# Kernel tuning notes

Measured on AMD Instinct MI355X. Metric: run time of the kernel, lower is better.

Reference implementation:

```python
import jax, jax.numpy as jnp
import numpy as np

N_BINS = 15
NUM_CLASSES = 16


def _risk_from_H2(u):
    # torch: 0.5*(1 - sqrt(clamp(2*2^-u - 1, min=0)))
    inner = 2.0 * jnp.exp2(-u) - 1.0
    pos = inner > 0.0
    s = jnp.sqrt(jnp.where(pos, inner, 1.0))  # safe sqrt (grad 0 where clamped)
    return 0.5 * (1.0 - jnp.where(pos, s, 0.0))


def setup_inputs() -> dict:
    key = jax.random.key(0)
    k1, k2 = jax.random.split(key)
    N = 4194304
    logits = jax.random.normal(k1, (N, NUM_CLASSES), dtype=jnp.float32)
    labels = jax.random.randint(k2, (N,), 0, NUM_CLASSES)
    return {"logits": logits, "labels": labels}


def reference(logits, labels):
    # logits: [N, C]; labels: [N]
    probs = jax.nn.softmax(logits, axis=-1)                     # [N, C]
    H2 = -jnp.log2((probs * probs).sum(-1) + 1e-12)             # [N]
    err_real = (jnp.argmax(probs, axis=-1) != labels).astype(H2.dtype)  # [N]

    # equal-frequency edges on detached H2 (linear-interp quantiles, as torch.quantile)
    q = jnp.linspace(0.0, 1.0, N_BINS + 1)
    edges = jnp.quantile(jax.lax.stop_gradient(H2), q)
    edges = edges.at[-1].add(1e-6)
    lo, hi = edges[:-1], edges[1:]                              # [n_bins]

    # vectorized replacement of the per-bin Python loop: [n_bins, N] mask
    mask = (H2[None, :] > lo[:, None]) & (H2[None, :] <= hi[:, None])
    maskf = mask.astype(H2.dtype)
    cnt = maskf.sum(-1)                                         # [n_bins]
    safe = jnp.maximum(cnt, 1.0)
    u_bar = (maskf @ H2) / safe                                 # masked means
    err_bar = (maskf @ err_real) / safe
    gaps = jnp.where(cnt > 0.0, jnp.abs(err_bar - _risk_from_H2(u_bar)), 0.0)
    return gaps.mean()
```

## Files before the change

kernel.cpp:

```cpp
#include <hip/hip_runtime.h>

#define L1_BINS 8192
#define L2_BINS 512
#define KEY_MAX 4194303u
#define NH2_BLOCKS 512
#define NREF_BLOCKS 512
#define NBIN_BLOCKS 256

struct Ranks { unsigned int r[32]; };
struct Fracs { float f[16]; };

__global__ __launch_bounds__(256) void k_zero(uint4* __restrict__ p, int n4) {
  int i = blockIdx.x * blockDim.x + threadIdx.x;
  if (i < n4) p[i] = make_uint4(0u, 0u, 0u, 0u);
}

__global__ __launch_bounds__(256) void k_h2(const float* __restrict__ logits,
                                            const int* __restrict__ labels,
                                            unsigned int* __restrict__ keys,
                                            unsigned int* __restrict__ merged,
                                            int n) {
  __shared__ unsigned int lh[L1_BINS];
  for (int i = threadIdx.x; i < L1_BINS; i += blockDim.x) lh[i] = 0u;
  __syncthreads();
  int tid = blockIdx.x * blockDim.x + threadIdx.x;
  int sub = tid & 3;
  int group = tid >> 2;
  int ngroups = (gridDim.x * blockDim.x) >> 2;
  for (int row = group; row < n; row += ngroups) {
    float4 v = reinterpret_cast<const float4*>(logits)[(size_t)row * 4 + sub];
    float m = v.x; int a = 0;
    if (v.y > m) { m = v.y; a = 1; }
    if (v.z > m) { m = v.z; a = 2; }
    if (v.w > m) { m = v.w; a = 3; }
    int gidx = sub * 4 + a;
#pragma unroll
    for (int mask = 1; mask <= 2; mask <<= 1) {
      float om = __shfl_xor(m, mask);
      int oi = __shfl_xor(gidx, mask);
      if (om > m || (om == m && oi < gidx)) { m = om; gidx = oi; }
    }
    float e0 = __expf(v.x - m), e1 = __expf(v.y - m);
    float e2 = __expf(v.z - m), e3 = __expf(v.w - m);
    float Z = e0 + e1 + e2 + e3;
    float S2 = e0 * e0 + e1 * e1 + e2 * e2 + e3 * e3;
#pragma unroll
    for (int mask = 1; mask <= 2; mask <<= 1) {
      Z += __shfl_xor(Z, mask);
      S2 += __shfl_xor(S2, mask);
    }
    if (sub == 0) {
      float r = S2 / (Z * Z) + 1e-12f;
      float h2 = -__log2f(r);
      int ki = (int)(h2 * 1048576.0f);
      unsigned int key = (unsigned int)min(max(ki, 0), (int)KEY_MAX);
      unsigned int err = (gidx != labels[row]) ? 0x80000000u : 0u;
      keys[row] = key | err;
      atomicAdd(&lh[key >> 9], 1u);
    }
  }
  __syncthreads();
  for (int i = threadIdx.x; i < L1_BINS; i += blockDim.x) {
    unsigned int v = lh[i];
    if (v) atomicAdd(&merged[i], v);
  }
}

__global__ void k_select(const unsigned int* __restrict__ hist,
                         unsigned int* __restrict__ selpfx,
                         unsigned int* __restrict__ selrank,
                         float* __restrict__ vout,
                         int nb, int perq, int shift, int last, int first,
                         Ranks rk) {
  int j = blockIdx.x;
  int lane = threadIdx.x;
  const unsigned int* h = hist + (perq ? (size_t)j * (size_t)nb : (size_t)0);
  unsigned int rem = first ? rk.r[j] : selrank[j];
  int base = 0, len = nb;
  while (len > 64) {
    int chunk = (len + 63) >> 6;
    int start = base + lane * chunk;
    int end = base + len;
    unsigned int s = 0;
    for (int t = 0; t < chunk; ++t) {
      int idx = start + t;
      if (idx < end) s += h[idx];
    }
    unsigned int inc = s;
#pragma unroll
    for (int d = 1; d < 64; d <<= 1) {
      unsigned int u = __shfl_up(inc, d);
      if (lane >= d) inc += u;
    }
    unsigned int ex = inc - s;
    bool own = (rem >= ex) && (rem < ex + s);
    unsigned long long bal = __ballot(own);
    int src = __ffsll((long long)bal) - 1;
    unsigned int exs = __shfl(ex, src);
    int nbase = base + src * chunk;
    len = min(chunk, end - nbase);
    base = nbase;
    rem -= exs;
  }
  unsigned int s = (lane < len) ? h[base + lane] : 0u;
  unsigned int inc = s;
#pragma unroll
  for (int d = 1; d < 64; d <<= 1) {
    unsigned int u = __shfl_up(inc, d);
    if (lane >= d) inc += u;
  }
  unsigned int ex = inc - s;
  bool own = (rem >= ex) && (rem < ex + s);
  unsigned long long bal = __ballot(own);
  int src = __ffsll((long long)bal) - 1;
  unsigned int exs = __shfl(ex, src);
  if (lane == 0) {
    unsigned int idx = (unsigned int)(base + src);
    unsigned int pfx = first ? idx : ((selpfx[j] << shift) | idx);
    selpfx[j] = pfx;
    selrank[j] = rem - exs;
    if (last) vout[j] = __uint_as_float(pfx);
  }
}

__global__ __launch_bounds__(256) void k_refine(const unsigned int* __restrict__ keys,
                                                const unsigned int* __restrict__ selpfx,
                                                unsigned int* __restrict__ hist2,
                                                int n) {
  __shared__ unsigned int sp[32];
  if (threadIdx.x < 32) sp[threadIdx.x] = selpfx[threadIdx.x];
  __syncthreads();
  int stride = gridDim.x * blockDim.x;
  for (int i = blockIdx.x * blockDim.x + threadIdx.x; i < n; i += stride) {
    unsigned int key = keys[i] & KEY_MAX;
    unsigned int hi = key >> 9;
    unsigned int sub = key & (L2_BINS - 1);
#pragma unroll
    for (int jj = 0; jj < 32; ++jj) {
      if (hi == sp[jj]) atomicAdd(&hist2[jj * L2_BINS + (int)sub], 1u);
    }
  }
}

__global__ __launch_bounds__(256) void k_bin(const unsigned int* __restrict__ keys,
                                             const float* __restrict__ vp,
                                             float* __restrict__ partials,
                                             unsigned int* __restrict__ done,
                                             float* __restrict__ out, int n,
                                             Fracs fr) {
  __shared__ float sedge[16];
  __shared__ float swacc[4][48];
  __shared__ unsigned int is_last;
  if (threadIdx.x < 16) {
    int i = threadIdx.x;
    unsigned int klo = __float_as_uint(vp[2 * i]);
    unsigned int khi = __float_as_uint(vp[2 * i + 1]);
    float lo = (float)(klo + 1u) * 0x1p-20f;
    float hi = (float)(khi + 1u) * 0x1p-20f;
    float f = fr.f[i];
    float e = lo * (1.0f - f) + hi * f;
    if (i == 15) e += 1e-6f;
    sedge[i] = e;
  }
  __syncthreads();
  float e[16];
#pragma unroll
  for (int j = 0; j < 16; ++j) e[j] = sedge[j];
  float cnt[15], sH[15], sE[15];
#pragma unroll
  for (int b = 0; b < 15; ++b) { cnt[b] = 0.f; sH[b] = 0.f; sE[b] = 0.f; }
  int stride = gridDim.x * blockDim.x;
  for (int i = blockIdx.x * blockDim.x + threadIdx.x; i < n; i += stride) {
    unsigned int kp = keys[i];
    float h = ((float)(kp & KEY_MAX) + 0.5f) * 0x1p-20f;
    float er = (kp & 0x80000000u) ? 1.0f : 0.0f;
    int less = 0;
#pragma unroll
    for (int j = 0; j < 16; ++j) less += (h > e[j]) ? 1 : 0;
    int bin = less - 1;
#pragma unroll
    for (int b = 0; b < 15; ++b) {
      bool m = (bin == b);
      cnt[b] += m ? 1.f : 0.f;
      sH[b] += m ? h : 0.f;
      sE[b] += m ? er : 0.f;
    }
  }
  int wid = threadIdx.x >> 6;
  int lane = threadIdx.x & 63;
#pragma unroll
  for (int b = 0; b < 15; ++b) {
    float c = cnt[b], a = sH[b], s = sE[b];
    for (int off = 32; off > 0; off >>= 1) {
      c += __shfl_xor(c, off);
      a += __shfl_xor(a, off);
      s += __shfl_xor(s, off);
    }
    if (lane == 0) {
      swacc[wid][b] = c;
      swacc[wid][15 + b] = a;
      swacc[wid][30 + b] = s;
    }
  }
  __syncthreads();
  if (threadIdx.x < 45) {
    int v = threadIdx.x;
    float s = swacc[0][v] + swacc[1][v] + swacc[2][v] + swacc[3][v];
    partials[v * NBIN_BLOCKS + blockIdx.x] = s;
  }
  __threadfence();
  if (threadIdx.x == 0)
    is_last = (atomicAdd(done, 1u) == (unsigned int)gridDim.x - 1u) ? 1u : 0u;
  __syncthreads();
  if (is_last && threadIdx.x < 64) {
    __shared__ float sacc[45];
    int l = threadIdx.x;
    for (int v = 0; v < 45; ++v) {
      float s = 0.f;
      for (int b = l; b < NBIN_BLOCKS; b += 64) s += partials[v * NBIN_BLOCKS + b];
      for (int off = 32; off > 0; off >>= 1) s += __shfl_xor(s, off);
      if (l == 0) sacc[v] = s;
    }
    __builtin_amdgcn_s_barrier();
    float g = 0.f;
    if (l < 15) {
      float c = sacc[l], sh = sacc[15 + l], se = sacc[30 + l];
      float safe = fmaxf(c, 1.f);
      float u = sh / safe, eb = se / safe;
      float inner = 2.0f * exp2f(-u) - 1.0f;
      float s = (inner > 0.f) ? sqrtf(inner) : 0.f;
      float risk = 0.5f * (1.0f - s);
      g = (c > 0.f) ? fabsf(eb - risk) : 0.f;
    }
    for (int off = 32; off > 0; off >>= 1) g += __shfl_xor(g, off);
    if (l == 0) out[0] = g * (1.0f / 15.0f);
  }
}

extern "C" void kernel_launch(void* const* d_in, const int* in_sizes, int n_in,
                              void* d_out, int out_size, void* d_ws, size_t ws_size,
                              hipStream_t stream) {
  const float* logits = (const float*)d_in[0];
  const int* labels = (const int*)d_in[1];
  float* out = (float*)d_out;
  int n = in_sizes[1];

  char* ws = (char*)d_ws;
  size_t offKeys = 0;
  size_t offMerged = (size_t)n * 4;
  size_t offH2b = offMerged + (size_t)L1_BINS * 4;
  size_t offDone = offH2b + 32 * L2_BINS * 4;
  size_t zeroEnd = offDone + 16;
  size_t offSelP = zeroEnd;
  size_t offSelR = offSelP + 128;
  size_t offV = offSelR + 128;
  size_t offPart = (offV + 128 + 255) & ~(size_t)255;

  unsigned int* keys = (unsigned int*)(ws + offKeys);
  unsigned int* merged = (unsigned int*)(ws + offMerged);
  unsigned int* hist2 = (unsigned int*)(ws + offH2b);
  unsigned int* done = (unsigned int*)(ws + offDone);
  unsigned int* selp = (unsigned int*)(ws + offSelP);
  unsigned int* selr = (unsigned int*)(ws + offSelR);
  float* vp = (float*)(ws + offV);
  float* part = (float*)(ws + offPart);

  Ranks rk;
  Fracs fr;
  float nm1 = (float)(n - 1);
  for (int i = 0; i < 16; ++i) {
    float q = (i == 15) ? 1.0f : (float)i * (1.0f / 15.0f);
    float idxf = q * nm1;
    float flo = floorf(idxf);
    unsigned int klo = (unsigned int)flo;
    unsigned int khi = (unsigned int)ceilf(idxf);
    unsigned int maxi = (unsigned int)(n - 1);
    if (klo > maxi) klo = maxi;
    if (khi > maxi) khi = maxi;
    rk.r[2 * i] = klo;
    rk.r[2 * i + 1] = khi;
    fr.f[i] = idxf - flo;
  }

  int zero4 = (int)((zeroEnd - offMerged) >> 4);
  k_zero<<<(zero4 + 255) / 256, 256, 0, stream>>>((uint4*)(ws + offMerged), zero4);
  k_h2<<<NH2_BLOCKS, 256, 0, stream>>>(logits, labels, keys, merged, n);
  k_select<<<32, 64, 0, stream>>>(merged, selp, selr, vp, L1_BINS, 0, 0, 0, 1, rk);
  k_refine<<<NREF_BLOCKS, 256, 0, stream>>>(keys, selp, hist2, n);
  k_select<<<32, 64, 0, stream>>>(hist2, selp, selr, vp, L2_BINS, 1, 9, 1, 0, rk);
  k_bin<<<NBIN_BLOCKS, 256, 0, stream>>>(keys, vp, part, done, out, n, fr);

  (void)n_in; (void)out_size; (void)ws_size;
}
```

Measured before the change: 330.7 us.

## Write per-block packed histograms and merge in a separate kernel instead of atomics

The H2 kernel now writes each block's 8192-bin local histogram as packed 16-bit pairs to a per-block slice of global memory, instead of merging it into a shared global histogram with atomics. A new merge kernel sums these slices column-wise to build the merged histogram. The grid grows from 512 to 1280 blocks to raise occupancy for the streaming pass, and the zero-fill no longer covers the merged histogram. The change adds about 20 MB of extra writes and reads plus one more launch. The 16-bit packing assumes no bin in one block exceeds 65535 counts, which holds because each block handles only about 3277 rows.

```diff
diff --git a/kernel.cpp b/kernel.cpp
--- a/kernel.cpp
+++ b/kernel.cpp
@@ -3,7 +3,7 @@
 #define L1_BINS 8192
 #define L2_BINS 512
 #define KEY_MAX 4194303u
-#define NH2_BLOCKS 512
+#define NH2_BLOCKS 1280
 #define NREF_BLOCKS 512
 #define NBIN_BLOCKS 256
 
@@ -18,7 +18,7 @@
 __global__ __launch_bounds__(256) void k_h2(const float* __restrict__ logits,
                                             const int* __restrict__ labels,
                                             unsigned int* __restrict__ keys,
-                                            unsigned int* __restrict__ merged,
+                                            unsigned int* __restrict__ histg,
                                             int n) {
   __shared__ unsigned int lh[L1_BINS];
   for (int i = threadIdx.x; i < L1_BINS; i += blockDim.x) lh[i] = 0u;
@@ -60,9 +60,34 @@
     }
   }
   __syncthreads();
-  for (int i = threadIdx.x; i < L1_BINS; i += blockDim.x) {
-    unsigned int v = lh[i];
-    if (v) atomicAdd(&merged[i], v);
+  unsigned int* dst = histg + (size_t)blockIdx.x * (L1_BINS / 2);
+  for (int i = threadIdx.x; i < L1_BINS / 2; i += blockDim.x)
+    dst[i] = (lh[2 * i] & 0xFFFFu) | (lh[2 * i + 1] << 16);
+}
+
+__global__ __launch_bounds__(256) void k_merge(const unsigned int* __restrict__ histg,
+                                               unsigned int* __restrict__ merged,
+                                               int nrows) {
+  __shared__ unsigned int slo[16][17], shi[16][17];
+  int col0 = blockIdx.x * 16;
+  int c = threadIdx.x & 15;
+  int rg = threadIdx.x >> 4;
+  unsigned int alo = 0, ahi = 0;
+  for (int r = rg; r < nrows; r += 16) {
+    unsigned int v = histg[(size_t)r * (L1_BINS / 2) + col0 + c];
+    alo += v & 0xFFFFu;
+    ahi += v >> 16;
+  }
+  slo[rg][c] = alo;
+  shi[rg][c] = ahi;
+  __syncthreads();
+  if (threadIdx.x < 16) {
+    unsigned int lo = 0, hi = 0;
+#pragma unroll
+    for (int g = 0; g < 16; ++g) { lo += slo[g][threadIdx.x]; hi += shi[g][threadIdx.x]; }
+    int pc = col0 + threadIdx.x;
+    merged[2 * pc] = lo;
+    merged[2 * pc + 1] = hi;
   }
 }
 
@@ -247,7 +272,8 @@
 
   char* ws = (char*)d_ws;
   size_t offKeys = 0;
-  size_t offMerged = (size_t)n * 4;
+  size_t offHg = (size_t)n * 4;
+  size_t offMerged = offHg + (size_t)NH2_BLOCKS * (L1_BINS / 2) * 4;
   size_t offH2b = offMerged + (size_t)L1_BINS * 4;
   size_t offDone = offH2b + 32 * L2_BINS * 4;
   size_t zeroEnd = offDone + 16;
@@ -257,6 +283,7 @@
   size_t offPart = (offV + 128 + 255) & ~(size_t)255;
 
   unsigned int* keys = (unsigned int*)(ws + offKeys);
+  unsigned int* histg = (unsigned int*)(ws + offHg);
   unsigned int* merged = (unsigned int*)(ws + offMerged);
   unsigned int* hist2 = (unsigned int*)(ws + offH2b);
   unsigned int* done = (unsigned int*)(ws + offDone);
@@ -282,9 +309,10 @@
     fr.f[i] = idxf - flo;
   }
 
-  int zero4 = (int)((zeroEnd - offMerged) >> 4);
-  k_zero<<<(zero4 + 255) / 256, 256, 0, stream>>>((uint4*)(ws + offMerged), zero4);
-  k_h2<<<NH2_BLOCKS, 256, 0, stream>>>(logits, labels, keys, merged, n);
+  int zero4 = (int)((zeroEnd - offH2b) >> 4);
+  k_zero<<<(zero4 + 255) / 256, 256, 0, stream>>>((uint4*)(ws + offH2b), zero4);
+  k_h2<<<NH2_BLOCKS, 256, 0, stream>>>(logits, labels, keys, histg, n);
+  k_merge<<<L1_BINS / 2 / 16, 256, 0, stream>>>(histg, merged, NH2_BLOCKS);
   k_select<<<32, 64, 0, stream>>>(merged, selp, selr, vp, L1_BINS, 0, 0, 0, 1, rk);
   k_refine<<<NREF_BLOCKS, 256, 0, stream>>>(keys, selp, hist2, n);
   k_select<<<32, 64, 0, stream>>>(hist2, selp, selr, vp, L2_BINS, 1, 9, 1, 0, rk);
```

Result: faster. 317.1 us (-4.1%).
